# Optimization experiments

Measured on AMD Instinct MI355X. Metric: run time of the kernel, lower is better.

## Reference

```python
import jax, jax.numpy as jnp
import numpy as np
from functools import partial

U = 1200   # thought_size (GRU units)
E = 620    # word_size
V = 20000  # vocab_size
B = 128    # batch
T = 64     # seq_len
LN_EPS = 1e-3  # Keras LayerNormalization default epsilon


def layernorm(x, gamma, beta, eps=LN_EPS):
    m = jnp.mean(x, axis=-1, keepdims=True)
    v = jnp.mean(jnp.square(x - m), axis=-1, keepdims=True)
    return gamma * (x - m) * jax.lax.rsqrt(v + eps) + beta


def gru_ln_direction(emb, kernel, rkernel, bias, ln0_g, ln0_b, ln3_g, ln3_b):
    """Run the LayerNorm-GRU (impl=2, reset_after=True) over emb [B,T,E].
    Returns final hidden state [B,U]."""
    input_bias, recurrent_bias = bias[0], bias[1]
    # Time-parallel input projection: [B,T,3U]
    x_proj = jnp.einsum('bte,eu->btu', emb, kernel) + input_bias
    x_proj_t = jnp.transpose(x_proj, (1, 0, 2))  # [T,B,3U]

    def step(h, xt):
        h_ln = layernorm(h, ln0_g, ln0_b)                      # LN on previous state
        inner = h_ln @ rkernel + recurrent_bias                # [B,3U]
        z = jax.nn.sigmoid(xt[:, :U] + inner[:, :U])
        r = jax.nn.sigmoid(xt[:, U:2 * U] + inner[:, U:2 * U])
        rec_h = r * inner[:, 2 * U:]
        hh = jnp.tanh(layernorm(xt[:, 2 * U:] + rec_h, ln3_g, ln3_b))
        h_new = z * h_ln + (1.0 - z) * hh
        return h_new, None

    h0 = jnp.zeros((emb.shape[0], U), dtype=emb.dtype)
    h_final, _ = jax.lax.scan(step, h0, x_proj_t)
    return h_final


def setup_inputs() -> dict:
    key = jax.random.key(0)
    ks = jax.random.split(key, 8)
    s = 0.05
    return {
        'sentences': jax.random.randint(ks[0], (B, T), 0, V),
        'embed': jax.random.normal(ks[1], (V, E), jnp.float32) * s,
        'fw_kernel': jax.random.normal(ks[2], (E, 3 * U), jnp.float32) * s,
        'fw_rkernel': jax.random.normal(ks[3], (U, 3 * U), jnp.float32) * s,
        'fw_bias': jax.random.normal(ks[4], (2, 3 * U), jnp.float32) * s,
        'fw_ln0_g': jnp.ones((U,), jnp.float32),
        'fw_ln0_b': jnp.zeros((U,), jnp.float32),
        'fw_ln3_g': jnp.ones((U,), jnp.float32),
        'fw_ln3_b': jnp.zeros((U,), jnp.float32),
        'bw_kernel': jax.random.normal(ks[5], (E, 3 * U), jnp.float32) * s,
        'bw_rkernel': jax.random.normal(ks[6], (U, 3 * U), jnp.float32) * s,
        'bw_bias': jax.random.normal(ks[7], (2, 3 * U), jnp.float32) * s,
        'bw_ln0_g': jnp.ones((U,), jnp.float32),
        'bw_ln0_b': jnp.zeros((U,), jnp.float32),
        'bw_ln3_g': jnp.ones((U,), jnp.float32),
        'bw_ln3_b': jnp.zeros((U,), jnp.float32),
    }


def reference(sentences, embed, fw_kernel, fw_rkernel, fw_bias,
              fw_ln0_g, fw_ln0_b, fw_ln3_g, fw_ln3_b,
              bw_kernel, bw_rkernel, bw_bias,
              bw_ln0_g, bw_ln0_b, bw_ln3_g, bw_ln3_b):
    embedding = jnp.tanh(embed[sentences])  # [B,T,E]
    forward_h = gru_ln_direction(embedding, fw_kernel, fw_rkernel, fw_bias,
                                 fw_ln0_g, fw_ln0_b, fw_ln3_g, fw_ln3_b)
    backward_h = gru_ln_direction(embedding[:, ::-1, :], bw_kernel, bw_rkernel, bw_bias,
                                  bw_ln0_g, bw_ln0_b, bw_ln3_g, bw_ln3_b)
    thought_vector = jnp.concatenate([forward_h, backward_h], axis=1)  # [B,2U]
    return thought_vector, embedding
```

## Files before the change

kernel.cpp:

```cpp
#include <hip/hip_runtime.h>
#include <hip/hip_bf16.h>

#define U_    1200
#define E_    620
#define B_    128
#define T_    64
#define N3    3600
#define NP    3712
#define KE    640
#define KU    1216
#define WIN   16
#define LN_EPS 1e-3f

typedef __attribute__((ext_vector_type(8))) short short8;
typedef __attribute__((ext_vector_type(4))) float f32x4;

constexpr size_t OFF_EMBH  = 0;
constexpr size_t SZ_EMB    = (size_t)8192 * KE * 2;
constexpr size_t OFF_EMBL  = OFF_EMBH + SZ_EMB;
constexpr size_t OFF_KTH   = OFF_EMBL + SZ_EMB;
constexpr size_t SZ_KT     = (size_t)2 * NP * KE * 2;
constexpr size_t OFF_KTL   = OFF_KTH + SZ_KT;
constexpr size_t OFF_RKTH  = OFF_KTL + SZ_KT;
constexpr size_t SZ_RKT    = (size_t)2 * NP * KU * 2;
constexpr size_t OFF_RKTL  = OFF_RKTH + SZ_RKT;
constexpr size_t OFF_XPWH  = OFF_RKTL + SZ_RKT;
constexpr size_t SZ_XPW    = (size_t)2 * WIN * B_ * NP * 2;
constexpr size_t OFF_XPWL  = OFF_XPWH + SZ_XPW;
constexpr size_t OFF_INNER = OFF_XPWL + SZ_XPW;
constexpr size_t SZ_INNER  = (size_t)4 * B_ * NP * 4;
constexpr size_t OFF_HLN   = OFF_INNER + SZ_INNER;
constexpr size_t SZ_HLN    = (size_t)2 * B_ * U_ * 4;
constexpr size_t OFF_HLNBH = OFF_HLN + SZ_HLN;
constexpr size_t SZ_HLNB   = (size_t)2 * B_ * KU * 2;
constexpr size_t OFF_HLNBL = OFF_HLNBH + SZ_HLNB;

__device__ inline void lds_load16(const void* g, void* l) {
  __builtin_amdgcn_global_load_lds(
      (const __attribute__((address_space(1))) unsigned int*)g,
      (__attribute__((address_space(3))) unsigned int*)l, 16, 0, 0);
}

__device__ inline float sigmf(float x) { return 1.f / (1.f + expf(-x)); }

__global__ __launch_bounds__(256)
void embed_kernel(const int* __restrict__ sent, const float* __restrict__ embed,
                  float* __restrict__ out_emb,
                  __hip_bfloat16* __restrict__ embH, __hip_bfloat16* __restrict__ embL) {
  const int row = blockIdx.x;
  const int idx = sent[row];
  const float* src = embed + (size_t)idx * E_;
  for (int e = threadIdx.x; e < KE; e += 256) {
    float v = 0.f;
    if (e < E_) {
      v = tanhf(src[e]);
      out_emb[(size_t)row * E_ + e] = v;
    }
    const __hip_bfloat16 hi = __float2bfloat16(v);
    embH[(size_t)row * KE + e] = hi;
    embL[(size_t)row * KE + e] = __float2bfloat16(v - __bfloat162float(hi));
  }
}

__global__ __launch_bounds__(256)
void transpose_cast(const float* __restrict__ W0, const float* __restrict__ W1,
                    __hip_bfloat16* __restrict__ WtHi, __hip_bfloat16* __restrict__ WtLo,
                    int Kreal, int Kp) {
  const int d = blockIdx.z;
  const float* W = d ? W1 : W0;
  __hip_bfloat16* dstH = WtHi + (size_t)d * NP * Kp;
  __hip_bfloat16* dstL = WtLo + (size_t)d * NP * Kp;
  __shared__ float tile[32][33];
  const int n0 = blockIdx.x * 32, k0 = blockIdx.y * 32;
  const int tx = threadIdx.x, ty = threadIdx.y;
#pragma unroll
  for (int i = 0; i < 32; i += 8) {
    const int k = k0 + ty + i, n = n0 + tx;
    tile[ty + i][tx] = (k < Kreal && n < N3) ? W[(size_t)k * N3 + n] : 0.f;
  }
  __syncthreads();
#pragma unroll
  for (int i = 0; i < 32; i += 8) {
    const int n = n0 + ty + i, k = k0 + tx;
    const float v = tile[tx][ty + i];
    const __hip_bfloat16 hi = __float2bfloat16(v);
    dstH[(size_t)n * Kp + k] = hi;
    dstL[(size_t)n * Kp + k] = __float2bfloat16(v - __bfloat162float(hi));
  }
}

__global__ __launch_bounds__(256)
void init_hln(const float* __restrict__ fw_b0, const float* __restrict__ bw_b0,
              float* __restrict__ hln, __hip_bfloat16* __restrict__ hlnbH,
              __hip_bfloat16* __restrict__ hlnbL) {
  const int idx = blockIdx.x * 256 + threadIdx.x;
  if (idx >= 2 * B_ * KU) return;
  const int k = idx % KU;
  const int rowd = idx / KU;
  const int d = rowd >> 7;
  float v = 0.f;
  if (k < U_) {
    v = (d ? bw_b0 : fw_b0)[k];
    hln[(size_t)rowd * U_ + k] = v;
  }
  const __hip_bfloat16 hi = __float2bfloat16(v);
  hlnbH[idx] = hi;
  hlnbL[idx] = __float2bfloat16(v - __bfloat162float(hi));
}

__global__ __launch_bounds__(256)
void xwin_gemm(const __hip_bfloat16* __restrict__ embH, const __hip_bfloat16* __restrict__ embL,
               const __hip_bfloat16* __restrict__ kTH, const __hip_bfloat16* __restrict__ kTL,
               const float* __restrict__ fw_bias, const float* __restrict__ bw_bias,
               __hip_bfloat16* __restrict__ xpwH, __hip_bfloat16* __restrict__ xpwL,
               int w0) {
  constexpr int BM = 128, BN = 128, BK = 64;
  constexpr int WM = 64, WN = 64, FM = 4, FN = 4;
  constexpr int TA = BM * BK, TB = BN * BK;
  const int d = blockIdx.z;
  const __hip_bfloat16* BH = kTH + (size_t)d * NP * KE;
  const __hip_bfloat16* BL = kTL + (size_t)d * NP * KE;

  const int m0 = blockIdx.y * BM;
  const int n0 = blockIdx.x * BN;
  const int tid = threadIdx.x;
  const int lane = tid & 63;
  const int wid = tid >> 6;
  const int wr = wid >> 1, wc = wid & 1;

  __shared__ __align__(16) __hip_bfloat16 As[2 * TA];
  __shared__ __align__(16) __hip_bfloat16 Bs[2 * TB];

  f32x4 acc[FM][FN] = {};

  const int srow = tid >> 3;
  const int scol = (tid & 7) << 3;

  for (int ks = 0; ks < KE / BK; ++ks) {
    const int k0 = ks * BK;
    __syncthreads();
#pragma unroll
    for (int it = 0; it < TA / 2048; ++it) {
      const int row = m0 + it * 32 + srow;
      const int b = row & 127, srel = row >> 7;
      const int txi = d ? (T_ - 1 - (w0 + srel)) : (w0 + srel);
      const size_t goff = (size_t)(b * T_ + txi) * KE + k0 + scol;
      lds_load16(embH + goff, As + it * 2048 + tid * 8);
      lds_load16(embL + goff, As + TA + it * 2048 + tid * 8);
    }
#pragma unroll
    for (int it = 0; it < TB / 2048; ++it) {
      const size_t goff = (size_t)(n0 + it * 32 + srow) * KE + k0 + scol;
      lds_load16(BH + goff, Bs + it * 2048 + tid * 8);
      lds_load16(BL + goff, Bs + TB + it * 2048 + tid * 8);
    }
    __syncthreads();
#pragma unroll
    for (int kk = 0; kk < BK / 32; ++kk) {
      short8 ah[FM], al[FM], bh[FN], bl[FN];
#pragma unroll
      for (int mi = 0; mi < FM; ++mi) {
        const int off = (wr * WM + mi * 16 + (lane & 15)) * BK + kk * 32 + (lane >> 4) * 8;
        ah[mi] = *(const short8*)(As + off);
        al[mi] = *(const short8*)(As + TA + off);
      }
#pragma unroll
      for (int ni = 0; ni < FN; ++ni) {
        const int off = (wc * WN + ni * 16 + (lane & 15)) * BK + kk * 32 + (lane >> 4) * 8;
        bh[ni] = *(const short8*)(Bs + off);
        bl[ni] = *(const short8*)(Bs + TB + off);
      }
#pragma unroll
      for (int mi = 0; mi < FM; ++mi)
#pragma unroll
        for (int ni = 0; ni < FN; ++ni) {
          acc[mi][ni] = __builtin_amdgcn_mfma_f32_16x16x32_bf16(ah[mi], bh[ni], acc[mi][ni], 0, 0, 0);
          acc[mi][ni] = __builtin_amdgcn_mfma_f32_16x16x32_bf16(ah[mi], bl[ni], acc[mi][ni], 0, 0, 0);
          acc[mi][ni] = __builtin_amdgcn_mfma_f32_16x16x32_bf16(al[mi], bh[ni], acc[mi][ni], 0, 0, 0);
        }
    }
  }

  const float* ib = d ? bw_bias : fw_bias;
#pragma unroll
  for (int mi = 0; mi < FM; ++mi)
#pragma unroll
    for (int ni = 0; ni < FN; ++ni) {
      const int gc = n0 + wc * WN + ni * 16 + (lane & 15);
      const float bv = (gc < N3) ? ib[gc] : 0.f;
      const int gr0 = m0 + wr * WM + mi * 16 + ((lane >> 4) << 2);
#pragma unroll
      for (int j = 0; j < 4; ++j) {
        const int gr = gr0 + j;
        const int b = gr & 127, srel = gr >> 7;
        const size_t off = ((size_t)(d * WIN + srel) * B_ + b) * NP + gc;
        const float v = acc[mi][ni][j] + bv;
        const __hip_bfloat16 hi = __float2bfloat16(v);
        xpwH[off] = hi;
        xpwL[off] = __float2bfloat16(v - __bfloat162float(hi));
      }
    }
}

__global__ __launch_bounds__(256)
void step_rec(const __hip_bfloat16* __restrict__ hlnbH, const __hip_bfloat16* __restrict__ hlnbL,
              const __hip_bfloat16* __restrict__ rkTH, const __hip_bfloat16* __restrict__ rkTL,
              float* __restrict__ inner) {
  constexpr int BM = 64, BN = 64, BK = 64;
  constexpr int WM = 32, WN = 32, FM = 2, FN = 2;
  constexpr int TA = BM * BK, TB = BN * BK;
  const int z = blockIdx.z;
  const int d = z >> 1, kp = z & 1;
  const int ks0 = kp ? 10 : 0;
  const int ks1 = kp ? 19 : 10;

  const __hip_bfloat16* BH = rkTH + (size_t)d * NP * KU;
  const __hip_bfloat16* BL = rkTL + (size_t)d * NP * KU;

  const int m0 = blockIdx.y * BM;
  const int n0 = blockIdx.x * BN;
  const int tid = threadIdx.x;
  const int lane = tid & 63;
  const int wid = tid >> 6;
  const int wr = wid >> 1, wc = wid & 1;

  __shared__ __align__(16) __hip_bfloat16 As[2 * TA];
  __shared__ __align__(16) __hip_bfloat16 Bs[2 * TB];

  f32x4 acc[FM][FN] = {};

  const int srow = tid >> 3;
  const int scol = (tid & 7) << 3;

  for (int ks = ks0; ks < ks1; ++ks) {
    const int k0 = ks * BK;
    __syncthreads();
#pragma unroll
    for (int it = 0; it < TA / 2048; ++it) {
      const int row = m0 + it * 32 + srow;
      const size_t goff = (size_t)(d * B_ + row) * KU + k0 + scol;
      lds_load16(hlnbH + goff, As + it * 2048 + tid * 8);
      lds_load16(hlnbL + goff, As + TA + it * 2048 + tid * 8);
    }
#pragma unroll
    for (int it = 0; it < TB / 2048; ++it) {
      const size_t goff = (size_t)(n0 + it * 32 + srow) * KU + k0 + scol;
      lds_load16(BH + goff, Bs + it * 2048 + tid * 8);
      lds_load16(BL + goff, Bs + TB + it * 2048 + tid * 8);
    }
    __syncthreads();
#pragma unroll
    for (int kk = 0; kk < BK / 32; ++kk) {
      short8 ah[FM], al[FM], bh[FN], bl[FN];
#pragma unroll
      for (int mi = 0; mi < FM; ++mi) {
        const int off = (wr * WM + mi * 16 + (lane & 15)) * BK + kk * 32 + (lane >> 4) * 8;
        ah[mi] = *(const short8*)(As + off);
        al[mi] = *(const short8*)(As + TA + off);
      }
#pragma unroll
      for (int ni = 0; ni < FN; ++ni) {
        const int off = (wc * WN + ni * 16 + (lane & 15)) * BK + kk * 32 + (lane >> 4) * 8;
        bh[ni] = *(const short8*)(Bs + off);
        bl[ni] = *(const short8*)(Bs + TB + off);
      }
#pragma unroll
      for (int mi = 0; mi < FM; ++mi)
#pragma unroll
        for (int ni = 0; ni < FN; ++ni) {
          acc[mi][ni] = __builtin_amdgcn_mfma_f32_16x16x32_bf16(ah[mi], bh[ni], acc[mi][ni], 0, 0, 0);
          acc[mi][ni] = __builtin_amdgcn_mfma_f32_16x16x32_bf16(ah[mi], bl[ni], acc[mi][ni], 0, 0, 0);
          acc[mi][ni] = __builtin_amdgcn_mfma_f32_16x16x32_bf16(al[mi], bh[ni], acc[mi][ni], 0, 0, 0);
          acc[mi][ni] = __builtin_amdgcn_mfma_f32_16x16x32_bf16(al[mi], bl[ni], acc[mi][ni], 0, 0, 0);
        }
    }
  }

  float* C = inner + (size_t)z * B_ * NP;
#pragma unroll
  for (int mi = 0; mi < FM; ++mi)
#pragma unroll
    for (int ni = 0; ni < FN; ++ni) {
      const int gc = n0 + wc * WN + ni * 16 + (lane & 15);
      const int gr = m0 + wr * WM + mi * 16 + ((lane >> 4) << 2);
#pragma unroll
      for (int j = 0; j < 4; ++j)
        C[(size_t)(gr + j) * NP + gc] = acc[mi][ni][j];
    }
}

__device__ inline void breduce2(float& a, float& b, float* red, int tid) {
#pragma unroll
  for (int off = 32; off; off >>= 1) {
    a += __shfl_down(a, off, 64);
    b += __shfl_down(b, off, 64);
  }
  const int w = tid >> 6;
  __syncthreads();
  if ((tid & 63) == 0) { red[w] = a; red[4 + w] = b; }
  __syncthreads();
  a = red[0] + red[1] + red[2] + red[3];
  b = red[4] + red[5] + red[6] + red[7];
}

__global__ __launch_bounds__(256)
void gru_update(const float* __restrict__ inner,
                const __hip_bfloat16* __restrict__ xpwH, const __hip_bfloat16* __restrict__ xpwL,
                const float* __restrict__ fw_bias, const float* __restrict__ bw_bias,
                const float* __restrict__ fw_ln0g, const float* __restrict__ fw_ln0b,
                const float* __restrict__ fw_ln3g, const float* __restrict__ fw_ln3b,
                const float* __restrict__ bw_ln0g, const float* __restrict__ bw_ln0b,
                const float* __restrict__ bw_ln3g, const float* __restrict__ bw_ln3b,
                float* __restrict__ hln, __hip_bfloat16* __restrict__ hlnbH,
                __hip_bfloat16* __restrict__ hlnbL,
                float* __restrict__ out_tv, int srel, int t) {
  const int bid = blockIdx.x;
  const int d = bid >> 7;
  const int r = bid & 127;
  const int tid = threadIdx.x;

  const float* rec0 = inner + ((size_t)(d * 2 + 0) * B_ + r) * NP;
  const float* rec1 = inner + ((size_t)(d * 2 + 1) * B_ + r) * NP;
  const size_t xoff = ((size_t)(d * WIN + srel) * B_ + r) * NP;
  const __hip_bfloat16* xH = xpwH + xoff;
  const __hip_bfloat16* xL = xpwL + xoff;
  const float* rb = (d ? bw_bias : fw_bias) + N3;
  const float* g0 = d ? bw_ln0g : fw_ln0g;
  const float* b0 = d ? bw_ln0b : fw_ln0b;
  const float* g3 = d ? bw_ln3g : fw_ln3g;
  const float* b3 = d ? bw_ln3b : fw_ln3b;
  float* hl = hln + ((size_t)d * B_ + r) * U_;
  __hip_bfloat16* hlbH = hlnbH + ((size_t)d * B_ + r) * KU;
  __hip_bfloat16* hlbL = hlnbL + ((size_t)d * B_ + r) * KU;

  __shared__ float red[8];

  float zv[5], cv[5], hv[5];
  float s1 = 0.f, s2 = 0.f;
#pragma unroll
  for (int i = 0; i < 5; ++i) {
    const int c = tid + i * 256;
    if (c < U_) {
      const float xz = __bfloat162float(xH[c]) + __bfloat162float(xL[c]);
      const float xg = __bfloat162float(xH[U_ + c]) + __bfloat162float(xL[U_ + c]);
      const float xh = __bfloat162float(xH[2 * U_ + c]) + __bfloat162float(xL[2 * U_ + c]);
      const float z  = sigmf(xz + rec0[c] + rec1[c] + rb[c]);
      const float rr = sigmf(xg + rec0[U_ + c] + rec1[U_ + c] + rb[U_ + c]);
      const float cand = xh + rr * (rec0[2 * U_ + c] + rec1[2 * U_ + c] + rb[2 * U_ + c]);
      zv[i] = z; cv[i] = cand;
      s1 += cand; s2 += cand * cand;
    }
  }
  breduce2(s1, s2, red, tid);
  const float m1 = s1 / U_;
  const float is1 = rsqrtf(s2 / U_ - m1 * m1 + LN_EPS);

  float t1 = 0.f, t2 = 0.f;
#pragma unroll
  for (int i = 0; i < 5; ++i) {
    const int c = tid + i * 256;
    if (c < U_) {
      const float hh = tanhf(g3[c] * (cv[i] - m1) * is1 + b3[c]);
      const float hn = zv[i] * hl[c] + (1.f - zv[i]) * hh;
      hv[i] = hn;
      t1 += hn; t2 += hn * hn;
    }
  }
  breduce2(t1, t2, red, tid);
  const float m2 = t1 / U_;
  const float is2 = rsqrtf(t2 / U_ - m2 * m2 + LN_EPS);

#pragma unroll
  for (int i = 0; i < 5; ++i) {
    const int c = tid + i * 256;
    if (c < U_) {
      const float hlnew = g0[c] * (hv[i] - m2) * is2 + b0[c];
      hl[c] = hlnew;
      const __hip_bfloat16 hi = __float2bfloat16(hlnew);
      hlbH[c] = hi;
      hlbL[c] = __float2bfloat16(hlnew - __bfloat162float(hi));
      if (t == T_ - 1) out_tv[(size_t)r * 2400 + (size_t)d * U_ + c] = hv[i];
    }
  }
}

extern "C" void kernel_launch(void* const* d_in, const int* in_sizes, int n_in,
                              void* d_out, int out_size, void* d_ws, size_t ws_size,
                              hipStream_t stream) {
  const int*   sent      = (const int*)  d_in[0];
  const float* embed     = (const float*)d_in[1];
  const float* fw_kernel = (const float*)d_in[2];
  const float* fw_rkern  = (const float*)d_in[3];
  const float* fw_bias   = (const float*)d_in[4];
  const float* fw_ln0g   = (const float*)d_in[5];
  const float* fw_ln0b   = (const float*)d_in[6];
  const float* fw_ln3g   = (const float*)d_in[7];
  const float* fw_ln3b   = (const float*)d_in[8];
  const float* bw_kernel = (const float*)d_in[9];
  const float* bw_rkern  = (const float*)d_in[10];
  const float* bw_bias   = (const float*)d_in[11];
  const float* bw_ln0g   = (const float*)d_in[12];
  const float* bw_ln0b   = (const float*)d_in[13];
  const float* bw_ln3g   = (const float*)d_in[14];
  const float* bw_ln3b   = (const float*)d_in[15];

  uint8_t* ws = (uint8_t*)d_ws;
  __hip_bfloat16* embH  = (__hip_bfloat16*)(ws + OFF_EMBH);
  __hip_bfloat16* embL  = (__hip_bfloat16*)(ws + OFF_EMBL);
  __hip_bfloat16* kTH   = (__hip_bfloat16*)(ws + OFF_KTH);
  __hip_bfloat16* kTL   = (__hip_bfloat16*)(ws + OFF_KTL);
  __hip_bfloat16* rkTH  = (__hip_bfloat16*)(ws + OFF_RKTH);
  __hip_bfloat16* rkTL  = (__hip_bfloat16*)(ws + OFF_RKTL);
  __hip_bfloat16* xpwH  = (__hip_bfloat16*)(ws + OFF_XPWH);
  __hip_bfloat16* xpwL  = (__hip_bfloat16*)(ws + OFF_XPWL);
  float*          inner = (float*)(ws + OFF_INNER);
  float*          hln   = (float*)(ws + OFF_HLN);
  __hip_bfloat16* hlnbH = (__hip_bfloat16*)(ws + OFF_HLNBH);
  __hip_bfloat16* hlnbL = (__hip_bfloat16*)(ws + OFF_HLNBL);

  float* out_tv  = (float*)d_out;
  float* out_emb = (float*)d_out + (size_t)B_ * 2 * U_;

  embed_kernel<<<B_ * T_, 256, 0, stream>>>(sent, embed, out_emb, embH, embL);

  transpose_cast<<<dim3(NP / 32, KE / 32, 2), dim3(32, 8), 0, stream>>>(
      fw_kernel, bw_kernel, kTH, kTL, E_, KE);
  transpose_cast<<<dim3(NP / 32, KU / 32, 2), dim3(32, 8), 0, stream>>>(
      fw_rkern, bw_rkern, rkTH, rkTL, U_, KU);

  init_hln<<<(2 * B_ * KU + 255) / 256, 256, 0, stream>>>(fw_ln0b, bw_ln0b,
                                                          hln, hlnbH, hlnbL);

  for (int w0 = 0; w0 < T_; w0 += WIN) {
    xwin_gemm<<<dim3(NP / 128, (WIN * B_) / 128, 2), 256, 0, stream>>>(
        embH, embL, kTH, kTL, fw_bias, bw_bias, xpwH, xpwL, w0);
    for (int s = 0; s < WIN; ++s) {
      const int t = w0 + s;
      step_rec<<<dim3(NP / 64, B_ / 64, 4), 256, 0, stream>>>(
          hlnbH, hlnbL, rkTH, rkTL, inner);
      gru_update<<<2 * B_, 256, 0, stream>>>(
          inner, xpwH, xpwL, fw_bias, bw_bias,
          fw_ln0g, fw_ln0b, fw_ln3g, fw_ln3b,
          bw_ln0g, bw_ln0b, bw_ln3g, bw_ln3b,
          hln, hlnbH, hlnbL, out_tv, s, t);
    }
  }
}
```

Baseline: 2.071 ms.

## Split recurrent GEMM K four ways, double-buffer weights, swizzle LDS, remap blocks

```diff
diff --git a/kernel.cpp b/kernel.cpp
--- a/kernel.cpp
+++ b/kernel.cpp
@@ -28,7 +28,7 @@
 constexpr size_t SZ_XPW    = (size_t)2 * WIN * B_ * NP * 2;
 constexpr size_t OFF_XPWL  = OFF_XPWH + SZ_XPW;
 constexpr size_t OFF_INNER = OFF_XPWL + SZ_XPW;
-constexpr size_t SZ_INNER  = (size_t)4 * B_ * NP * 4;
+constexpr size_t SZ_INNER  = (size_t)8 * B_ * NP * 4;
 constexpr size_t OFF_HLN   = OFF_INNER + SZ_INNER;
 constexpr size_t SZ_HLN    = (size_t)2 * B_ * U_ * 4;
 constexpr size_t OFF_HLNBH = OFF_HLN + SZ_HLN;
@@ -108,6 +108,13 @@
   hlnbL[idx] = __float2bfloat16(v - __bfloat162float(hi));
 }
 
+__device__ inline int swz_scol(int tid) {
+  return (((tid & 7) ^ ((tid >> 3) & 7)) << 3);
+}
+__device__ inline int swz_off(int row, int kk, int lane) {
+  return row * 64 + ((kk * 32 + ((lane >> 4) << 3)) ^ ((row & 7) << 3));
+}
+
 __global__ __launch_bounds__(256)
 void xwin_gemm(const __hip_bfloat16* __restrict__ embH, const __hip_bfloat16* __restrict__ embL,
                const __hip_bfloat16* __restrict__ kTH, const __hip_bfloat16* __restrict__ kTL,
@@ -117,12 +124,17 @@
   constexpr int BM = 128, BN = 128, BK = 64;
   constexpr int WM = 64, WN = 64, FM = 4, FN = 4;
   constexpr int TA = BM * BK, TB = BN * BK;
-  const int d = blockIdx.z;
+  const int bid = blockIdx.x;
+  const int w = (bid & 7) * 116 + (bid >> 3);
+  const int d = w / 464;
+  const int q = w % 464;
+  const int nt = q / 16, mt = q % 16;
+  const int m0 = mt * BM;
+  const int n0 = nt * BN;
+
   const __hip_bfloat16* BH = kTH + (size_t)d * NP * KE;
   const __hip_bfloat16* BL = kTL + (size_t)d * NP * KE;
 
-  const int m0 = blockIdx.y * BM;
-  const int n0 = blockIdx.x * BN;
   const int tid = threadIdx.x;
   const int lane = tid & 63;
   const int wid = tid >> 6;
@@ -134,7 +146,7 @@
   f32x4 acc[FM][FN] = {};
 
   const int srow = tid >> 3;
-  const int scol = (tid & 7) << 3;
+  const int scol = swz_scol(tid);
 
   for (int ks = 0; ks < KE / BK; ++ks) {
     const int k0 = ks * BK;
@@ -160,13 +172,15 @@
       short8 ah[FM], al[FM], bh[FN], bl[FN];
 #pragma unroll
       for (int mi = 0; mi < FM; ++mi) {
-        const int off = (wr * WM + mi * 16 + (lane & 15)) * BK + kk * 32 + (lane >> 4) * 8;
+        const int row = wr * WM + mi * 16 + (lane & 15);
+        const int off = swz_off(row, kk, lane);
         ah[mi] = *(const short8*)(As + off);
         al[mi] = *(const short8*)(As + TA + off);
       }
 #pragma unroll
       for (int ni = 0; ni < FN; ++ni) {
-        const int off = (wc * WN + ni * 16 + (lane & 15)) * BK + kk * 32 + (lane >> 4) * 8;
+        const int row = wc * WN + ni * 16 + (lane & 15);
+        const int off = swz_off(row, kk, lane);
         bh[ni] = *(const short8*)(Bs + off);
         bl[ni] = *(const short8*)(Bs + TB + off);
       }
@@ -206,86 +220,96 @@
 void step_rec(const __hip_bfloat16* __restrict__ hlnbH, const __hip_bfloat16* __restrict__ hlnbL,
               const __hip_bfloat16* __restrict__ rkTH, const __hip_bfloat16* __restrict__ rkTL,
               float* __restrict__ inner) {
-  constexpr int BM = 64, BN = 64, BK = 64;
-  constexpr int WM = 32, WN = 32, FM = 2, FN = 2;
-  constexpr int TA = BM * BK, TB = BN * BK;
-  const int z = blockIdx.z;
-  const int d = z >> 1, kp = z & 1;
-  const int ks0 = kp ? 10 : 0;
-  const int ks1 = kp ? 19 : 10;
-
-  const __hip_bfloat16* BH = rkTH + (size_t)d * NP * KU;
-  const __hip_bfloat16* BL = rkTL + (size_t)d * NP * KU;
-
-  const int m0 = blockIdx.y * BM;
-  const int n0 = blockIdx.x * BN;
+  const int bid = blockIdx.x;
+  const int w = (bid & 7) * 116 + (bid >> 3);
+  const int m  = w & 1;
+  const int q  = w >> 1;
+  const int nt = q % 58;
+  const int z  = q / 58;
+  const int d  = z >> 2, kp = z & 3;
+  const int ks0 = kp * 5;
+  const int ks1 = (kp == 3) ? 19 : (ks0 + 5);
+  const int n0 = nt * 64;
+  const int m0 = m * 64;
+
   const int tid = threadIdx.x;
   const int lane = tid & 63;
   const int wid = tid >> 6;
   const int wr = wid >> 1, wc = wid & 1;
 
-  __shared__ __align__(16) __hip_bfloat16 As[2 * TA];
-  __shared__ __align__(16) __hip_bfloat16 Bs[2 * TB];
-
-  f32x4 acc[FM][FN] = {};
+  const __hip_bfloat16* WH = rkTH + (size_t)d * NP * KU;
+  const __hip_bfloat16* WL = rkTL + (size_t)d * NP * KU;
+
+  __shared__ __align__(16) __hip_bfloat16 Bs[2][2][4096];
 
   const int srow = tid >> 3;
-  const int scol = (tid & 7) << 3;
-
+  const int scol = swz_scol(tid);
+
+  const size_t arow0 = (size_t)(d * B_ + m0 + wr * 32 + (lane & 15)) * KU + ((lane >> 4) << 3);
+
+  f32x4 acc[2][2] = {};
+
+#define STAGE_B(buf, ks)                                                       \
+  {                                                                            \
+    const size_t kc = (size_t)(ks) * 64 + scol;                                \
+    _Pragma("unroll")                                                          \
+    for (int it = 0; it < 2; ++it) {                                           \
+      const size_t g = (size_t)(n0 + it * 32 + srow) * KU + kc;                \
+      lds_load16(WH + g, &Bs[buf][0][it * 2048 + tid * 8]);                    \
+      lds_load16(WL + g, &Bs[buf][1][it * 2048 + tid * 8]);                    \
+    }                                                                          \
+  }
+
+  STAGE_B(0, ks0);
+  __syncthreads();
+  int cur = 0;
   for (int ks = ks0; ks < ks1; ++ks) {
-    const int k0 = ks * BK;
+    if (ks + 1 < ks1) STAGE_B(cur ^ 1, ks + 1);
+    const size_t ab = arow0 + (size_t)ks * 64;
+    short8 ah[2][2], al[2][2];
+#pragma unroll
+    for (int mi = 0; mi < 2; ++mi)
+#pragma unroll
+      for (int kk = 0; kk < 2; ++kk) {
+        const size_t a = ab + (size_t)mi * 16 * KU + kk * 32;
+        ah[mi][kk] = *(const short8*)(hlnbH + a);
+        al[mi][kk] = *(const short8*)(hlnbL + a);
+      }
+#pragma unroll
+    for (int kk = 0; kk < 2; ++kk) {
+      short8 bh[2], bl[2];
+#pragma unroll
+      for (int nf = 0; nf < 2; ++nf) {
+        const int row = wc * 32 + nf * 16 + (lane & 15);
+        const int off = swz_off(row, kk, lane);
+        bh[nf] = *(const short8*)(&Bs[cur][0][off]);
+        bl[nf] = *(const short8*)(&Bs[cur][1][off]);
+      }
+#pragma unroll
+      for (int mi = 0; mi < 2; ++mi)
+#pragma unroll
+        for (int nf = 0; nf < 2; ++nf) {
+          acc[mi][nf] = __builtin_amdgcn_mfma_f32_16x16x32_bf16(ah[mi][kk], bh[nf], acc[mi][nf], 0, 0, 0);
+          acc[mi][nf] = __builtin_amdgcn_mfma_f32_16x16x32_bf16(ah[mi][kk], bl[nf], acc[mi][nf], 0, 0, 0);
+          acc[mi][nf] = __builtin_amdgcn_mfma_f32_16x16x32_bf16(al[mi][kk], bh[nf], acc[mi][nf], 0, 0, 0);
+          acc[mi][nf] = __builtin_amdgcn_mfma_f32_16x16x32_bf16(al[mi][kk], bl[nf], acc[mi][nf], 0, 0, 0);
+        }
+    }
     __syncthreads();
-#pragma unroll
-    for (int it = 0; it < TA / 2048; ++it) {
-      const int row = m0 + it * 32 + srow;
-      const size_t goff = (size_t)(d * B_ + row) * KU + k0 + scol;
-      lds_load16(hlnbH + goff, As + it * 2048 + tid * 8);
-      lds_load16(hlnbL + goff, As + TA + it * 2048 + tid * 8);
-    }
-#pragma unroll
-    for (int it = 0; it < TB / 2048; ++it) {
-      const size_t goff = (size_t)(n0 + it * 32 + srow) * KU + k0 + scol;
-      lds_load16(BH + goff, Bs + it * 2048 + tid * 8);
-      lds_load16(BL + goff, Bs + TB + it * 2048 + tid * 8);
-    }
-    __syncthreads();
-#pragma unroll
-    for (int kk = 0; kk < BK / 32; ++kk) {
-      short8 ah[FM], al[FM], bh[FN], bl[FN];
-#pragma unroll
-      for (int mi = 0; mi < FM; ++mi) {
-        const int off = (wr * WM + mi * 16 + (lane & 15)) * BK + kk * 32 + (lane >> 4) * 8;
-        ah[mi] = *(const short8*)(As + off);
-        al[mi] = *(const short8*)(As + TA + off);
-      }
-#pragma unroll
-      for (int ni = 0; ni < FN; ++ni) {
-        const int off = (wc * WN + ni * 16 + (lane & 15)) * BK + kk * 32 + (lane >> 4) * 8;
-        bh[ni] = *(const short8*)(Bs + off);
-        bl[ni] = *(const short8*)(Bs + TB + off);
-      }
-#pragma unroll
-      for (int mi = 0; mi < FM; ++mi)
-#pragma unroll
-        for (int ni = 0; ni < FN; ++ni) {
-          acc[mi][ni] = __builtin_amdgcn_mfma_f32_16x16x32_bf16(ah[mi], bh[ni], acc[mi][ni], 0, 0, 0);
-          acc[mi][ni] = __builtin_amdgcn_mfma_f32_16x16x32_bf16(ah[mi], bl[ni], acc[mi][ni], 0, 0, 0);
-          acc[mi][ni] = __builtin_amdgcn_mfma_f32_16x16x32_bf16(al[mi], bh[ni], acc[mi][ni], 0, 0, 0);
-          acc[mi][ni] = __builtin_amdgcn_mfma_f32_16x16x32_bf16(al[mi], bl[ni], acc[mi][ni], 0, 0, 0);
-        }
-    }
-  }
+    cur ^= 1;
+  }
+#undef STAGE_B
 
   float* C = inner + (size_t)z * B_ * NP;
 #pragma unroll
-  for (int mi = 0; mi < FM; ++mi)
-#pragma unroll
-    for (int ni = 0; ni < FN; ++ni) {
-      const int gc = n0 + wc * WN + ni * 16 + (lane & 15);
-      const int gr = m0 + wr * WM + mi * 16 + ((lane >> 4) << 2);
+  for (int mi = 0; mi < 2; ++mi)
+#pragma unroll
+    for (int nf = 0; nf < 2; ++nf) {
+      const int gc = n0 + wc * 32 + nf * 16 + (lane & 15);
+      const int gr = m0 + wr * 32 + mi * 16 + ((lane >> 4) << 2);
 #pragma unroll
       for (int j = 0; j < 4; ++j)
-        C[(size_t)(gr + j) * NP + gc] = acc[mi][ni][j];
+        C[(size_t)(gr + j) * NP + gc] = acc[mi][nf][j];
     }
 }
 
@@ -319,8 +343,10 @@
   const int r = bid & 127;
   const int tid = threadIdx.x;
 
-  const float* rec0 = inner + ((size_t)(d * 2 + 0) * B_ + r) * NP;
-  const float* rec1 = inner + ((size_t)(d * 2 + 1) * B_ + r) * NP;
+  const float* rec0 = inner + ((size_t)(d * 4 + 0) * B_ + r) * NP;
+  const float* rec1 = inner + ((size_t)(d * 4 + 1) * B_ + r) * NP;
+  const float* rec2 = inner + ((size_t)(d * 4 + 2) * B_ + r) * NP;
+  const float* rec3 = inner + ((size_t)(d * 4 + 3) * B_ + r) * NP;
   const size_t xoff = ((size_t)(d * WIN + srel) * B_ + r) * NP;
   const __hip_bfloat16* xH = xpwH + xoff;
   const __hip_bfloat16* xL = xpwL + xoff;
@@ -344,9 +370,12 @@
       const float xz = __bfloat162float(xH[c]) + __bfloat162float(xL[c]);
       const float xg = __bfloat162float(xH[U_ + c]) + __bfloat162float(xL[U_ + c]);
       const float xh = __bfloat162float(xH[2 * U_ + c]) + __bfloat162float(xL[2 * U_ + c]);
-      const float z  = sigmf(xz + rec0[c] + rec1[c] + rb[c]);
-      const float rr = sigmf(xg + rec0[U_ + c] + rec1[U_ + c] + rb[U_ + c]);
-      const float cand = xh + rr * (rec0[2 * U_ + c] + rec1[2 * U_ + c] + rb[2 * U_ + c]);
+      const float rz = (rec0[c] + rec1[c]) + (rec2[c] + rec3[c]);
+      const float rg = (rec0[U_ + c] + rec1[U_ + c]) + (rec2[U_ + c] + rec3[U_ + c]);
+      const float rh = (rec0[2 * U_ + c] + rec1[2 * U_ + c]) + (rec2[2 * U_ + c] + rec3[2 * U_ + c]);
+      const float z  = sigmf(xz + rz + rb[c]);
+      const float rr = sigmf(xg + rg + rb[U_ + c]);
+      const float cand = xh + rr * (rh + rb[2 * U_ + c]);
       zv[i] = z; cv[i] = cand;
       s1 += cand; s2 += cand * cand;
     }
@@ -432,12 +461,11 @@
                                                           hln, hlnbH, hlnbL);
 
   for (int w0 = 0; w0 < T_; w0 += WIN) {
-    xwin_gemm<<<dim3(NP / 128, (WIN * B_) / 128, 2), 256, 0, stream>>>(
+    xwin_gemm<<<928, 256, 0, stream>>>(
         embH, embL, kTH, kTL, fw_bias, bw_bias, xpwH, xpwL, w0);
     for (int s = 0; s < WIN; ++s) {
       const int t = w0 + s;
-      step_rec<<<dim3(NP / 64, B_ / 64, 4), 256, 0, stream>>>(
-          hlnbH, hlnbL, rkTH, rkTL, inner);
+      step_rec<<<928, 256, 0, stream>>>(hlnbH, hlnbL, rkTH, rkTL, inner);
       gru_update<<<2 * B_, 256, 0, stream>>>(
           inner, xpwH, xpwL, fw_bias, bw_bias,
           fw_ln0g, fw_ln0b, fw_ln3g, fw_ln3b,
```

Measured after the change: 2.611 ms. 1.26x slower.
